# Kernel tuning notes

Hardware: AMD Instinct MI355X
Metric: run time of the kernel (lower is better)

## Reference

```python
import jax, jax.numpy as jnp
import numpy as np

KERNEL_SIZE = 11  # int(resolution / 11.6) with resolution=128
SIGMA = 1.5
K1, K2 = 0.01, 0.03


def gaussian_kernel(k=KERNEL_SIZE, sigma=SIGMA):
    coords = jnp.arange(k, dtype=jnp.float32) - (k - 1) / 2
    g = jnp.exp(-coords ** 2 / (2 * sigma ** 2))
    g = g / g.sum()
    return jnp.outer(g, g)  # (k,k)


def depthwise_conv(x, kern):
    # x: (N,C,H,W), kern: (k,k); depthwise (groups=C), SAME padding, stride 1
    C = x.shape[1]
    k = kern.shape[0]
    w = jnp.broadcast_to(kern[None, None], (C, 1, k, k))
    return jax.lax.conv_general_dilated(
        x, w, window_strides=(1, 1), padding='SAME',
        feature_group_count=C,
        dimension_numbers=('NCHW', 'OIHW', 'NCHW'))


def dssim_map(x, y, kern):
    C1, C2 = K1 ** 2, K2 ** 2
    mu_x = depthwise_conv(x, kern)
    mu_y = depthwise_conv(y, kern)
    sigma_x = depthwise_conv(x * x, kern) - mu_x ** 2
    sigma_y = depthwise_conv(y * y, kern) - mu_y ** 2
    sigma_xy = depthwise_conv(x * y, kern) - mu_x * mu_y
    ssim_num = (2 * mu_x * mu_y + C1) * (2 * sigma_xy + C2)
    ssim_den = (mu_x ** 2 + mu_y ** 2 + C1) * (sigma_x + sigma_y + C2)
    ssim = ssim_num / (ssim_den + 1e-8)
    return (1 - ssim) / 2  # (N,C,H,W)


def poly_mask(pts, H, W):
    # pts: (P,2) polygon vertices (x, y). Vectorized ray-casting point-in-polygon,
    # restricted to the truncated bounding box exactly like the torch code
    # (mask[:, :, ymin:ymax, xmin:xmax] slice), and zeroed if polygon exits frame.
    x, y = pts[:, 0], pts[:, 1]
    xmin, xmax = jnp.floor(x.min()), jnp.floor(x.max())  # == int() for positive coords
    ymin, ymax = jnp.floor(y.min()), jnp.floor(y.max())
    valid = (xmin >= 0) & (ymin >= 0) & (xmax < W) & (ymax < H)
    yy, xx = jnp.meshgrid(jnp.arange(H, dtype=jnp.float32),
                          jnp.arange(W, dtype=jnp.float32), indexing='ij')
    x1, y1 = x[:, None, None], y[:, None, None]        # (P,1,1)
    x2 = jnp.roll(x, -1)[:, None, None]
    y2 = jnp.roll(y, -1)[:, None, None]
    Y, X = yy[None], xx[None]                          # (1,H,W)
    cond = ((y1 > Y) != (y2 > Y)) & (X < (x2 - x1) * (Y - y1) / (y2 - y1 + 1e-6) + x1)
    inside = (cond.sum(axis=0) % 2) == 1               # XOR-fold over edges, (H,W)
    bbox = (yy >= ymin) & (yy < ymax) & (xx >= xmin) & (xx < xmax)
    return jnp.where(valid, (inside & bbox).astype(jnp.float32), 0.0)


def weight_map(lmrk, H, W):
    # lmrk: (68,2). weight = 1 + 3*eyeL + 3*eyeR + 2*mouth (additive, as in torch)
    return (1.0
            + 3.0 * poly_mask(lmrk[36:42], H, W)
            + 3.0 * poly_mask(lmrk[42:48], H, W)
            + 2.0 * poly_mask(lmrk[48:60], H, W))  # (H,W)


def setup_inputs() -> dict:
    key = jax.random.key(0)
    k1, k2, k3 = jax.random.split(key, 3)
    N, C, H, W = 48, 3, 256, 256
    pred = jax.random.normal(k1, (N, C, H, W), dtype=jnp.float32)
    target = jax.random.normal(k2, (N, C, H, W), dtype=jnp.float32)
    # landmarks strictly inside the frame so all polygons are rasterized
    landmarks = 20.0 + 216.0 * jax.random.uniform(k3, (N, 68, 2), dtype=jnp.float32)
    return {"pred": pred, "target": target, "landmarks": landmarks}


def reference(pred, target, landmarks):
    N, C, H, W = pred.shape
    kern = gaussian_kernel()
    # per-sample DSSIM (batch-of-1 conv in torch == batched conv here)
    d = dssim_map(pred, target, kern).mean(axis=(1, 2, 3))          # (N,)
    abs_diff = jnp.abs(pred - target)
    l1 = abs_diff.mean(axis=(1, 2, 3))                              # (N,)
    wmap = jax.vmap(lambda lm: weight_map(lm, H, W))(landmarks)     # (N,H,W)
    lw = (wmap[:, None] * abs_diff).mean(axis=(1, 2, 3))            # (N,)
    return (10.0 * d + 10.0 * l1 + 5.0 * lw).mean()
```

## Files before the change

kernel.cpp:

```cpp
#include <hip/hip_runtime.h>
#include <cmath>

#define HW 256
#define NIMG 48
#define NCH 3
#define NPLANE (NIMG * NCH)
#define STRIP 37
#define NSTRIP 7
#define NIN (STRIP + 10)
#define CHUNK 22
#define NCHUNK 3
#define NSLOT 64

__global__ void zero_ws_kernel(double* ws) {
    if (threadIdx.x < NSLOT) ws[threadIdx.x] = 0.0;
}

__launch_bounds__(256)
__global__ void fused_kernel(const float* __restrict__ pred,
                             const float* __restrict__ target,
                             const float* __restrict__ lmk,
                             double* __restrict__ ws)
{
    const int plane = blockIdx.x;
    const int n     = plane / 3;
    const int r0    = blockIdx.y * STRIP;
    const int x     = threadIdx.x;

    __shared__ float4 mva[2][HW + 10];
    __shared__ float  mvb[2][HW + 10];
    __shared__ float  sxc[STRIP][24];
    __shared__ int    srowflag[STRIP];
    __shared__ float  slm[48];
    __shared__ float  sbbs[12];
    __shared__ float  svalids[3];
    __shared__ float  red[12];

    float g6[6];
    {
        float gg[11]; float gs = 0.f;
#pragma unroll
        for (int q = 0; q < 11; ++q) {
            float c = (float)q - 5.0f;
            gg[q] = expf(-c * c / 4.5f);
            gs += gg[q];
        }
#pragma unroll
        for (int q = 0; q < 6; ++q) g6[q] = gg[q] / gs;
    }
#define GW(j) g6[(j) < 6 ? (j) : 10 - (j)]

    if (x < 48) slm[x] = lmk[n * 136 + 72 + x];
    if (x < 5) {
        const float4 z4 = make_float4(0.f, 0.f, 0.f, 0.f);
        mva[0][x] = z4; mva[0][261 + x] = z4;
        mva[1][x] = z4; mva[1][261 + x] = z4;
        mvb[0][x] = 0.f; mvb[0][261 + x] = 0.f;
        mvb[1][x] = 0.f; mvb[1][261 + x] = 0.f;
    }
    __syncthreads();

    if (x < 3) {
        const int s0 = (x == 0) ? 0 : (x == 1) ? 6 : 12;
        const int L  = (x == 2) ? 12 : 6;
        float xmn = 3e38f, xmx = -3e38f, ymn = 3e38f, ymx = -3e38f;
        for (int q = 0; q < L; ++q) {
            float px = slm[2 * (s0 + q)], py = slm[2 * (s0 + q) + 1];
            xmn = fminf(xmn, px); xmx = fmaxf(xmx, px);
            ymn = fminf(ymn, py); ymx = fmaxf(ymx, py);
        }
        xmn = floorf(xmn); xmx = floorf(xmx); ymn = floorf(ymn); ymx = floorf(ymx);
        sbbs[4 * x + 0] = xmn; sbbs[4 * x + 1] = xmx;
        sbbs[4 * x + 2] = ymn; sbbs[4 * x + 3] = ymx;
        svalids[x] = (xmn >= 0.f && ymn >= 0.f && xmx < 256.f && ymx < 256.f) ? 1.f : 0.f;
    }

#pragma unroll
    for (int u = 0; u < (STRIP * 24 + 255) / 256; ++u) {
        int idx = x + 256 * u;
        if (idx < STRIP * 24) {
            int r = idx / 24, e = idx - r * 24;
            float Y = (float)(r0 + r);
            const int s0 = (e < 6) ? 0 : (e < 12) ? 6 : 12;
            const int L  = (e < 12) ? 6 : 12;
            int il = e - s0;
            int i2 = (il + 1 == L) ? 0 : il + 1;
            float x1 = slm[2 * (s0 + il)], y1 = slm[2 * (s0 + il) + 1];
            float x2 = slm[2 * (s0 + i2)], y2 = slm[2 * (s0 + i2) + 1];
            bool crossing = (y1 > Y) != (y2 > Y);
            float xc = (x2 - x1) * (Y - y1) / (y2 - y1 + 1e-6f) + x1;
            sxc[r][e] = crossing ? xc : -3e38f;
        }
    }
    __syncthreads();

    if (x < STRIP) {
        float Y = (float)(r0 + x);
        int f = 0;
        if (svalids[0] != 0.f && Y >= sbbs[2]  && Y < sbbs[3])  f |= 1;
        if (svalids[1] != 0.f && Y >= sbbs[6]  && Y < sbbs[7])  f |= 2;
        if (svalids[2] != 0.f && Y >= sbbs[10] && Y < sbbs[11]) f |= 4;
        srowflag[x] = f;
    }
    __syncthreads();

    const float* __restrict__ pp = pred   + (size_t)plane * (HW * HW) + x;
    const float* __restrict__ tp = target + (size_t)plane * (HW * HW) + x;

    float rp[11], rt[11];
    float pfap, pfat, pfbp, pfbt;
    {
        int ra = r0 - 5;
        bool va = (ra >= 0);
        pfap = va ? pp[(size_t)ra * HW] : 0.f;
        pfat = va ? tp[(size_t)ra * HW] : 0.f;
        int rb = r0 - 4;
        bool vb = (rb >= 0);
        pfbp = vb ? pp[(size_t)rb * HW] : 0.f;
        pfbt = vb ? tp[(size_t)rb * HW] : 0.f;
    }

    float acc = 0.f, accl1 = 0.f, acclw = 0.f;
    const float X = (float)x;

    for (int c = 0; c < NCHUNK; ++c) {
#pragma unroll
        for (int t = 0; t < CHUNK; ++t) {
            const int i  = CHUNK * c + t;
            const int sr = t % 11;

            if (i < NIN) {
                if ((t & 1) == 0) { rp[sr] = pfap; rt[sr] = pfat; }
                else              { rp[sr] = pfbp; rt[sr] = pfbt; }
                {
                    int rin2 = r0 - 3 + i;
                    bool v = (i + 2 < NIN) && (rin2 >= 0) && (rin2 < HW);
                    float lp = 0.f, lt = 0.f;
                    if (v) {
                        lp = pp[(size_t)rin2 * HW];
                        lt = tp[(size_t)rin2 * HW];
                    }
                    if ((t & 1) == 0) { pfap = lp; pfat = lt; }
                    else              { pfbp = lp; pfbt = lt; }
                }

                if (i >= 5 && i < 5 + STRIP) {
                    int r_in = r0 - 5 + i;
                    if (r_in < HW) {
                        float ad = fabsf(rp[sr] - rt[sr]);
                        accl1 += ad;
                        float wgt = 1.f;
                        const int flags = srowflag[i - 5];
                        if (flags) {
                            const float* xc = sxc[i - 5];
                            int c0 = 0, c1 = 0, c2 = 0;
#pragma unroll
                            for (int e = 0; e < 6; ++e)   c0 += (X < xc[e]) ? 1 : 0;
#pragma unroll
                            for (int e = 6; e < 12; ++e)  c1 += (X < xc[e]) ? 1 : 0;
#pragma unroll
                            for (int e = 12; e < 24; ++e) c2 += (X < xc[e]) ? 1 : 0;
                            if ((flags & 1) && (c0 & 1) && X >= sbbs[0] && X < sbbs[1]) wgt += 3.f;
                            if ((flags & 2) && (c1 & 1) && X >= sbbs[4] && X < sbbs[5]) wgt += 3.f;
                            if ((flags & 4) && (c2 & 1) && X >= sbbs[8] && X < sbbs[9]) wgt += 2.f;
                        }
                        acclw += wgt * ad;
                    }
                }
            }

            if (i >= 10 && i < 10 + STRIP) {
                int r = r0 + i - 10;
                if (r < HW) {
                    float mux = 0.f, muy = 0.f, exx = 0.f, eyy = 0.f, exy = 0.f;
#pragma unroll
                    for (int j = 0; j < 11; ++j) {
                        const int s = (t + 1 + j) % 11;
                        float w = GW(j);
                        float p = rp[s], q = rt[s];
                        float wp = w * p, wt = w * q;
                        mux += wp; muy += wt;
                        exx = fmaf(wp, p, exx);
                        eyy = fmaf(wt, q, eyy);
                        exy = fmaf(wp, q, exy);
                    }
                    mva[t & 1][x + 5] = make_float4(mux, muy, exx, eyy);
                    mvb[t & 1][x + 5] = exy;
                }
            }

            if (i >= 11 && i < 11 + STRIP) {
                int rr = r0 + i - 11;
                if (rr < HW) {
                    const int b = (t + 1) & 1;
                    float Mx = 0.f, My = 0.f, Exx = 0.f, Eyy = 0.f, Exy = 0.f;
#pragma unroll
                    for (int k = 0; k < 11; ++k) {
                        float w = GW(k);
                        float4 m4 = mva[b][x + k];
                        float  m1 = mvb[b][x + k];
                        Mx  = fmaf(w, m4.x, Mx);
                        My  = fmaf(w, m4.y, My);
                        Exx = fmaf(w, m4.z, Exx);
                        Eyy = fmaf(w, m4.w, Eyy);
                        Exy = fmaf(w, m1,  Exy);
                    }
                    float sx  = Exx - Mx * Mx;
                    float sy  = Eyy - My * My;
                    float sxy = Exy - Mx * My;
                    const float C1 = 1e-4f, C2 = 9e-4f;
                    float num = (2.f * Mx * My + C1) * (2.f * sxy + C2);
                    float den = (Mx * Mx + My * My + C1) * (sx + sy + C2);
                    acc += 0.5f * (1.f - num / (den + 1e-8f));
                }
            }

            asm volatile("s_waitcnt lgkmcnt(0)" ::: "memory");
            __builtin_amdgcn_s_barrier();
        }
    }

#pragma unroll
    for (int off = 32; off > 0; off >>= 1) {
        acc   += __shfl_down(acc, off, 64);
        accl1 += __shfl_down(accl1, off, 64);
        acclw += __shfl_down(acclw, off, 64);
    }
    if ((x & 63) == 0) {
        int w = x >> 6;
        red[w] = acc; red[4 + w] = accl1; red[8 + w] = acclw;
    }
    __syncthreads();
    if (x == 0) {
        double s = 10.0 * ((double)red[0] + red[1] + red[2]  + red[3])
                 + 10.0 * ((double)red[4] + red[5] + red[6]  + red[7])
                 +  5.0 * ((double)red[8] + red[9] + red[10] + red[11]);
        atomicAdd(&ws[(blockIdx.y * NPLANE + blockIdx.x) & (NSLOT - 1)], s);
    }
}

__global__ void final_kernel(const double* __restrict__ ws, float* __restrict__ out) {
    double v = ws[threadIdx.x];
#pragma unroll
    for (int off = 32; off > 0; off >>= 1)
        v += __shfl_down(v, off, 64);
    if (threadIdx.x == 0) {
        const double denom = (double)NIMG * NCH * HW * HW;
        out[0] = (float)(v / denom);
    }
}

extern "C" void kernel_launch(void* const* d_in, const int* in_sizes, int n_in,
                              void* d_out, int out_size, void* d_ws, size_t ws_size,
                              hipStream_t stream)
{
    const float* pred   = (const float*)d_in[0];
    const float* target = (const float*)d_in[1];
    const float* lmk    = (const float*)d_in[2];
    float* out  = (float*)d_out;
    double* ws  = (double*)d_ws;

    hipLaunchKernelGGL(zero_ws_kernel, dim3(1), dim3(64), 0, stream, ws);
    hipLaunchKernelGGL(fused_kernel, dim3(NPLANE, NSTRIP), dim3(256), 0, stream,
                       pred, target, lmk, ws);
    hipLaunchKernelGGL(final_kernel, dim3(1), dim3(64), 0, stream, ws, out);
}
```

Measured before the change: 153.0 us.

## Shrink strips, pack pred/target into float2 vectors, fold final reduction into main kernel

Strips go from 37 rows in 7 blocks to 29 rows in 9 blocks per plane, giving more blocks for better occupancy at the cost of more halo rows re-read. Pred and target values are packed into 2-wide vectors so the compiler can emit packed FMA instructions. The separate final kernel is removed; the last block to finish, found through an atomic counter, does the final reduction, which saves one launch but adds a fence and an atomic in every block.

```diff
diff --git a/kernel.cpp b/kernel.cpp
--- a/kernel.cpp
+++ b/kernel.cpp
@@ -5,29 +5,34 @@
 #define NIMG 48
 #define NCH 3
 #define NPLANE (NIMG * NCH)
-#define STRIP 37
-#define NSTRIP 7
+#define STRIP 29
+#define NSTRIP 9
 #define NIN (STRIP + 10)
 #define CHUNK 22
-#define NCHUNK 3
+#define NCHUNK 2
 #define NSLOT 64
+#define NBLK (NPLANE * NSTRIP)
+
+typedef float f2 __attribute__((ext_vector_type(2)));
+typedef float f4 __attribute__((ext_vector_type(4)));
 
 __global__ void zero_ws_kernel(double* ws) {
-    if (threadIdx.x < NSLOT) ws[threadIdx.x] = 0.0;
+    if (threadIdx.x < NSLOT + 1) ws[threadIdx.x] = 0.0;
 }
 
 __launch_bounds__(256)
 __global__ void fused_kernel(const float* __restrict__ pred,
                              const float* __restrict__ target,
                              const float* __restrict__ lmk,
-                             double* __restrict__ ws)
+                             double* __restrict__ ws,
+                             float* __restrict__ out)
 {
     const int plane = blockIdx.x;
     const int n     = plane / 3;
     const int r0    = blockIdx.y * STRIP;
     const int x     = threadIdx.x;
 
-    __shared__ float4 mva[2][HW + 10];
+    __shared__ f4     mva[2][HW + 10];
     __shared__ float  mvb[2][HW + 10];
     __shared__ float  sxc[STRIP][24];
     __shared__ int    srowflag[STRIP];
@@ -35,6 +40,7 @@
     __shared__ float  sbbs[12];
     __shared__ float  svalids[3];
     __shared__ float  red[12];
+    __shared__ int    sdone;
 
     float g6[6];
     {
@@ -52,7 +58,7 @@
 
     if (x < 48) slm[x] = lmk[n * 136 + 72 + x];
     if (x < 5) {
-        const float4 z4 = make_float4(0.f, 0.f, 0.f, 0.f);
+        const f4 z4 = {0.f, 0.f, 0.f, 0.f};
         mva[0][x] = z4; mva[0][261 + x] = z4;
         mva[1][x] = z4; mva[1][261 + x] = z4;
         mvb[0][x] = 0.f; mvb[0][261 + x] = 0.f;
@@ -107,17 +113,17 @@
     const float* __restrict__ pp = pred   + (size_t)plane * (HW * HW) + x;
     const float* __restrict__ tp = target + (size_t)plane * (HW * HW) + x;
 
-    float rp[11], rt[11];
-    float pfap, pfat, pfbp, pfbt;
+    f2 ring[11];
+    f2 pfa, pfb;
     {
         int ra = r0 - 5;
         bool va = (ra >= 0);
-        pfap = va ? pp[(size_t)ra * HW] : 0.f;
-        pfat = va ? tp[(size_t)ra * HW] : 0.f;
+        pfa.x = va ? pp[(size_t)ra * HW] : 0.f;
+        pfa.y = va ? tp[(size_t)ra * HW] : 0.f;
         int rb = r0 - 4;
         bool vb = (rb >= 0);
-        pfbp = vb ? pp[(size_t)rb * HW] : 0.f;
-        pfbt = vb ? tp[(size_t)rb * HW] : 0.f;
+        pfb.x = vb ? pp[(size_t)rb * HW] : 0.f;
+        pfb.y = vb ? tp[(size_t)rb * HW] : 0.f;
     }
 
     float acc = 0.f, accl1 = 0.f, acclw = 0.f;
@@ -130,24 +136,25 @@
             const int sr = t % 11;
 
             if (i < NIN) {
-                if ((t & 1) == 0) { rp[sr] = pfap; rt[sr] = pfat; }
-                else              { rp[sr] = pfbp; rt[sr] = pfbt; }
+                if ((t & 1) == 0) ring[sr] = pfa;
+                else              ring[sr] = pfb;
                 {
                     int rin2 = r0 - 3 + i;
                     bool v = (i + 2 < NIN) && (rin2 >= 0) && (rin2 < HW);
-                    float lp = 0.f, lt = 0.f;
+                    f2 l = {0.f, 0.f};
                     if (v) {
-                        lp = pp[(size_t)rin2 * HW];
-                        lt = tp[(size_t)rin2 * HW];
-                    }
-                    if ((t & 1) == 0) { pfap = lp; pfat = lt; }
-                    else              { pfbp = lp; pfbt = lt; }
+                        l.x = pp[(size_t)rin2 * HW];
+                        l.y = tp[(size_t)rin2 * HW];
+                    }
+                    if ((t & 1) == 0) pfa = l;
+                    else              pfb = l;
                 }
 
                 if (i >= 5 && i < 5 + STRIP) {
                     int r_in = r0 - 5 + i;
                     if (r_in < HW) {
-                        float ad = fabsf(rp[sr] - rt[sr]);
+                        f2 pr = ring[sr];
+                        float ad = fabsf(pr.x - pr.y);
                         accl1 += ad;
                         float wgt = 1.f;
                         const int flags = srowflag[i - 5];
@@ -172,19 +179,21 @@
             if (i >= 10 && i < 10 + STRIP) {
                 int r = r0 + i - 10;
                 if (r < HW) {
-                    float mux = 0.f, muy = 0.f, exx = 0.f, eyy = 0.f, exy = 0.f;
+                    f2 mu = {0.f, 0.f};
+                    f2 sq = {0.f, 0.f};
+                    float exy = 0.f;
 #pragma unroll
                     for (int j = 0; j < 11; ++j) {
                         const int s = (t + 1 + j) % 11;
                         float w = GW(j);
-                        float p = rp[s], q = rt[s];
-                        float wp = w * p, wt = w * q;
-                        mux += wp; muy += wt;
-                        exx = fmaf(wp, p, exx);
-                        eyy = fmaf(wt, q, eyy);
-                        exy = fmaf(wp, q, exy);
-                    }
-                    mva[t & 1][x + 5] = make_float4(mux, muy, exx, eyy);
+                        f2 v  = ring[s];
+                        f2 wv = w * v;
+                        mu += wv;
+                        sq = __builtin_elementwise_fma(wv, v, sq);
+                        exy = fmaf(wv.x, v.y, exy);
+                    }
+                    f4 o; o.x = mu.x; o.y = mu.y; o.z = sq.x; o.w = sq.y;
+                    mva[t & 1][x + 5] = o;
                     mvb[t & 1][x + 5] = exy;
                 }
             }
@@ -193,24 +202,27 @@
                 int rr = r0 + i - 11;
                 if (rr < HW) {
                     const int b = (t + 1) & 1;
-                    float Mx = 0.f, My = 0.f, Exx = 0.f, Eyy = 0.f, Exy = 0.f;
+                    f2 M = {0.f, 0.f};
+                    f2 E = {0.f, 0.f};
+                    float Exy = 0.f;
 #pragma unroll
                     for (int k = 0; k < 11; ++k) {
                         float w = GW(k);
-                        float4 m4 = mva[b][x + k];
-                        float  m1 = mvb[b][x + k];
-                        Mx  = fmaf(w, m4.x, Mx);
-                        My  = fmaf(w, m4.y, My);
-                        Exx = fmaf(w, m4.z, Exx);
-                        Eyy = fmaf(w, m4.w, Eyy);
-                        Exy = fmaf(w, m1,  Exy);
-                    }
-                    float sx  = Exx - Mx * Mx;
-                    float sy  = Eyy - My * My;
-                    float sxy = Exy - Mx * My;
+                        f2 w2 = {w, w};
+                        f4 m4 = mva[b][x + k];
+                        f2 lo = {m4.x, m4.y};
+                        f2 hi = {m4.z, m4.w};
+                        float m1 = mvb[b][x + k];
+                        M = __builtin_elementwise_fma(w2, lo, M);
+                        E = __builtin_elementwise_fma(w2, hi, E);
+                        Exy = fmaf(w, m1, Exy);
+                    }
+                    float sx  = E.x - M.x * M.x;
+                    float sy  = E.y - M.y * M.y;
+                    float sxy = Exy - M.x * M.y;
                     const float C1 = 1e-4f, C2 = 9e-4f;
-                    float num = (2.f * Mx * My + C1) * (2.f * sxy + C2);
-                    float den = (Mx * Mx + My * My + C1) * (sx + sy + C2);
+                    float num = (2.f * M.x * M.y + C1) * (2.f * sxy + C2);
+                    float den = (M.x * M.x + M.y * M.y + C1) * (sx + sy + C2);
                     acc += 0.5f * (1.f - num / (den + 1e-8f));
                 }
             }
@@ -237,16 +249,24 @@
                  +  5.0 * ((double)red[8] + red[9] + red[10] + red[11]);
         atomicAdd(&ws[(blockIdx.y * NPLANE + blockIdx.x) & (NSLOT - 1)], s);
     }
-}
-
-__global__ void final_kernel(const double* __restrict__ ws, float* __restrict__ out) {
-    double v = ws[threadIdx.x];
-#pragma unroll
-    for (int off = 32; off > 0; off >>= 1)
-        v += __shfl_down(v, off, 64);
-    if (threadIdx.x == 0) {
-        const double denom = (double)NIMG * NCH * HW * HW;
-        out[0] = (float)(v / denom);
+
+    __threadfence();
+    if (x == 0) {
+        unsigned int old = atomicAdd((unsigned int*)(ws + NSLOT), 1u);
+        sdone = (old == (unsigned int)(NBLK - 1)) ? 1 : 0;
+    }
+    __syncthreads();
+    if (sdone) {
+        double v = (x < NSLOT) ? atomicAdd(&ws[x], 0.0) : 0.0;
+        if (x < 64) {
+#pragma unroll
+            for (int off = 32; off > 0; off >>= 1)
+                v += __shfl_down(v, off, 64);
+            if (x == 0) {
+                const double denom = (double)NIMG * NCH * HW * HW;
+                out[0] = (float)(v / denom);
+            }
+        }
     }
 }
 
@@ -260,8 +280,7 @@
     float* out  = (float*)d_out;
     double* ws  = (double*)d_ws;
 
-    hipLaunchKernelGGL(zero_ws_kernel, dim3(1), dim3(64), 0, stream, ws);
+    hipLaunchKernelGGL(zero_ws_kernel, dim3(1), dim3(128), 0, stream, ws);
     hipLaunchKernelGGL(fused_kernel, dim3(NPLANE, NSTRIP), dim3(256), 0, stream,
-                       pred, target, lmk, ws);
-    hipLaunchKernelGGL(final_kernel, dim3(1), dim3(64), 0, stream, ws, out);
+                       pred, target, lmk, ws, out);
 }
```

New measurement: 244.2 us. +59.6%, slower.
